# Performance work log

Hardware: AMD Instinct MI355X
Metric: run time of the kernel (lower is better)

## Reference

```python
import jax, jax.numpy as jnp
import numpy as np

# ---- fixed constants from stft2hcfp.__init__ ----
FS = 16000.0; FR = 2.0; FC = 27.5; TC = 1.0 / 4487.0; NPO = 48
N = int(FS / FR)                      # 8000 FFT length
HALF_N = int(round(N / 2))            # 4000
SQRT_N = float(np.sqrt(N))
HIGH_FREQ_IDX = int(round(1.0 / TC / FR) + 1)   # 2245
HIGH_QUEF_IDX = int(round(FS / FC)) + 1         # 583
CUT_Q = int(round(FS * TC))           # 4  (cepstrum cutoff)
TOTAL_BINS = 4 * 88                   # 352 log-freq bins
NUM_HARMONIC = 5

def _central_freqs():
    stop = 1.0 / TC
    nest = int(np.ceil(np.log2(stop / FC)) * NPO)
    cf = []
    for i in range(nest):
        c = FC * 2.0 ** (float(i) / NPO)
        if c < stop:
            cf.append(c)
        else:
            break
    return cf

CF = _central_freqs()   # 353 central frequencies
NEST = len(CF)

def _freq_matrix():
    # triangular log-frequency filterbank over linear freq axis
    f = (FS * np.linspace(0, 0.5, HALF_N, endpoint=True))[:HIGH_FREQ_IDX]
    W = np.zeros((NEST - 1, len(f)), np.float32)
    for i in range(1, NEST - 1):
        l = int(round(CF[i - 1] / FR)); r = int(round(CF[i + 1] / FR) + 1)
        if l >= r - 1:
            W[i, l] = 1.0
        else:
            for j in range(l, r):
                if CF[i - 1] < f[j] < CF[i]:
                    W[i, j] = (f[j] - CF[i - 1]) / (CF[i] - CF[i - 1])
                elif CF[i] < f[j] < CF[i + 1]:
                    W[i, j] = (CF[i + 1] - f[j]) / (CF[i + 1] - CF[i])
    return W

def _quef_matrix():
    q = np.arange(HIGH_QUEF_IDX) / FS + 1e-6
    fq = 1.0 / q
    W = np.zeros((NEST - 1, len(fq)), np.float32)
    for i in range(1, NEST - 1):
        for j in range(int(round(FS / CF[i + 1])), int(round(FS / CF[i - 1]) + 1)):
            if j >= len(fq):
                continue
            if CF[i - 1] < fq[j] < CF[i]:
                W[i, j] = (fq[j] - CF[i - 1]) / (CF[i] - CF[i - 1])
            elif CF[i] < fq[j] < CF[i + 1]:
                W[i, j] = (CF[i + 1] - fq[j]) / (CF[i + 1] - CF[i])
    return W

# harmonic shift indices: closest central freq to (k+1)*27.5 Hz, k=0..5
HIDS = [int(np.argmin(np.abs(np.asarray(CF) - (k + 1) * FC))) for k in range(NUM_HARMONIC + 1)]


def _nonlinear(x, g, cutoff):
    # relu + pow(g), then zero first/last `cutoff` rows along axis 1.
    # safe pow: grad is 0 where x<=0 (matches relu-masked torch behavior, no inf at 0)
    y = jnp.where(x > 0, jnp.where(x > 0, x, 1.0) ** g, 0.0)
    y = y.at[:, :cutoff].set(0.0).at[:, -cutoff:].set(0.0)
    return y


def setup_inputs() -> dict:
    key = jax.random.key(0)
    dx = jax.random.uniform(key, (8, 512, N), dtype=jnp.float32)  # [B, T, 8000] spectrogram
    return {
        "dx": dx,
        "W_freq": jnp.asarray(_freq_matrix()),   # [352, 2245]
        "W_quef": jnp.asarray(_quef_matrix()),   # [352, 583]
    }


def reference(dx, W_freq, W_quef):
    tfr0 = jnp.swapaxes(dx, 1, 2)                       # [B, F=8000, T]
    # CFP layer 1: real part of FFT over freq axis -> cepstrum, nonlinear g=0.6
    ceps = jnp.fft.fft(tfr0, axis=1).real / SQRT_N      # [B, 8000, T]
    ceps = _nonlinear(ceps, 0.6, CUT_Q)
    # log-frequency mappings (banded triangular filterbanks)
    tfr0h = tfr0[:, :HIGH_FREQ_IDX]                      # [B, 2245, T]
    cepsh = ceps[:, :HIGH_QUEF_IDX]                      # [B, 583, T]
    tfrL0 = jnp.einsum('kf,bft->bkt', W_freq, tfr0h)     # [B, 352, T]
    tfrLQ = jnp.einsum('kq,bqt->bkt', W_quef, cepsh)     # [B, 352, T]
    # harmonic stacking: shift down (spectral) / shift up (cepstral)
    har_s = [jnp.pad(tfrL0[:, h:TOTAL_BINS], ((0, 0), (0, h), (0, 0))) for h in HIDS]
    har_c = [jnp.pad(tfrLQ[:, :TOTAL_BINS - h], ((0, 0), (h, 0), (0, 0))) for h in HIDS]
    piece = jnp.concatenate([jnp.stack(har_s, axis=1), jnp.stack(har_c, axis=1)], axis=1)
    return jnp.swapaxes(piece, 2, 3)                     # [B, 12, T, 352]
```

## Files before the change

### kernel.cpp

```cpp
#include <hip/hip_runtime.h>
#include <hip/hip_bf16.h>
#include <limits.h>

typedef __attribute__((ext_vector_type(8))) short short8;
typedef __attribute__((ext_vector_type(4))) float f32x4;

#define NN 8000
#define NCOL 4096
#define KBINS 352
#define QPAD 640
#define QH 160
#define BN 128
#define KC 4
#define NTILE 125
#define CUTQ 4
#define T_ 512
#define WFB 64
#define WQB 20

#define GLL16(g, l) __builtin_amdgcn_global_load_lds( \
    (const __attribute__((address_space(1))) unsigned int*)(g), \
    (__attribute__((address_space(3))) unsigned int*)(l), 16, 0, 0)

static __device__ __forceinline__ ushort bfc(float f){
  __hip_bfloat16 h = __float2bfloat16(f);
  return *reinterpret_cast<ushort*>(&h);
}

__global__ void gen_cos_k(ushort* __restrict__ cosg, int HQI){
  int n = blockIdx.x*256 + threadIdx.x;
  int q = blockIdx.y;
  if (n >= NN) return;
  float v = 0.f;
  if (q < HQI){
    int m = (q*n) % NN;
    v = cosf((float)m * 7.8539816339744831e-4f);
  }
  int kt = n >> 6, s8 = (n >> 3) & 7, e = n & 7;
  cosg[(size_t)kt*(QPAD*64) + (size_t)q*64 + (((s8 ^ (q & 7)) << 3) | e)] = bfc(v);
}

__global__ void bounds_k(const float* __restrict__ W, int width,
                         int* __restrict__ lo, int* __restrict__ hi){
  __shared__ int slo, shi;
  int r = blockIdx.x;
  if (threadIdx.x==0){ slo = INT_MAX; shi = -1; }
  __syncthreads();
  int mylo = INT_MAX, myhi = -1;
  for (int c = threadIdx.x; c < width; c += 256){
    if (W[(size_t)r*width + c] != 0.f){ if (c < mylo) mylo = c; if (c > myhi) myhi = c; }
  }
  atomicMin(&slo, mylo); atomicMax(&shi, myhi);
  __syncthreads();
  if (threadIdx.x==0){
    if (shi < 0){ lo[r] = 0; hi[r] = 0; }
    else        { lo[r] = slo; hi[r] = shi + 1; }
  }
}

__global__ void pack_k(const float* __restrict__ W, const int* __restrict__ lo,
                       const int* __restrict__ hi, int width, int bw,
                       float* __restrict__ WT){
  int r = blockIdx.x;
  int l = lo[r], h = hi[r];
  for (int j = threadIdx.x; j < bw; j += 64){
    float v = 0.f;
    if (l + j < h) v = W[(size_t)r*width + l + j];
    WT[(size_t)j*KBINS + r] = v;
  }
}

__global__ __launch_bounds__(512, 4) void gemm_k(const float* __restrict__ dx,
                                                 const ushort* __restrict__ cosg,
                                                 float* __restrict__ part){
  __shared__ ushort As[2][QH*64];
  __shared__ ushort Bs[2][BN*64];
  int tid = threadIdx.x;
  int nb = blockIdx.x, qh = blockIdx.y, kc = blockIdx.z;
  int lane = tid & 63, widx = tid >> 6;
  int wm = widx & 1, wn = widx >> 1;
  int lrow = lane & 15, lk = lane >> 4;
  int kt0 = kc*32, ktE = (kt0 + 32 < NTILE) ? kt0 + 32 : NTILE;

  int brow = tid >> 2, bfo = (tid & 3) << 4;
  const float* dxp = dx + (size_t)(nb*BN + brow)*NN + bfo;
  int s8a = (tid & 3) << 1;
  const int bo0 = brow*64 + ((s8a ^ (brow & 7)) << 3);
  const int bo1 = brow*64 + (((s8a + 1) ^ (brow & 7)) << 3);
  const ushort* cg0 = cosg + (size_t)qh*(QH*64) + tid*8;

  f32x4 acc[5][2];
  #pragma unroll
  for (int a=0;a<5;a++){ acc[a][0] = (f32x4)0.f; acc[a][1] = (f32x4)0.f; }

  f32x4 d0,d1,d2,d3;
  {
    const float* p = dxp + (size_t)kt0*64;
    d0 = *(const f32x4*)p; d1 = *(const f32x4*)(p+4);
    d2 = *(const f32x4*)(p+8); d3 = *(const f32x4*)(p+12);
  }
  {
    const ushort* cg = cg0 + (size_t)kt0*(QPAD*64);
    GLL16(cg,        &As[0][tid*8]);
    GLL16(cg + 4096, &As[0][4096 + tid*8]);
    if (tid < 256) GLL16(cg + 8192, &As[0][8192 + tid*8]);
    short8 a8, b8;
    a8[0]=(short)bfc(d0[0]); a8[1]=(short)bfc(d0[1]); a8[2]=(short)bfc(d0[2]); a8[3]=(short)bfc(d0[3]);
    a8[4]=(short)bfc(d1[0]); a8[5]=(short)bfc(d1[1]); a8[6]=(short)bfc(d1[2]); a8[7]=(short)bfc(d1[3]);
    b8[0]=(short)bfc(d2[0]); b8[1]=(short)bfc(d2[1]); b8[2]=(short)bfc(d2[2]); b8[3]=(short)bfc(d2[3]);
    b8[4]=(short)bfc(d3[0]); b8[5]=(short)bfc(d3[1]); b8[6]=(short)bfc(d3[2]); b8[7]=(short)bfc(d3[3]);
    *(short8*)(&Bs[0][bo0]) = a8;
    *(short8*)(&Bs[0][bo1]) = b8;
    if (kt0 + 1 < ktE){
      const float* p = dxp + (size_t)(kt0+1)*64;
      d0 = *(const f32x4*)p; d1 = *(const f32x4*)(p+4);
      d2 = *(const f32x4*)(p+8); d3 = *(const f32x4*)(p+12);
    }
  }
  __syncthreads();

  int cur = 0;
  for (int kt = kt0; kt < ktE; ++kt){
    if (kt + 1 < ktE){
      const ushort* cg = cg0 + (size_t)(kt+1)*(QPAD*64);
      ushort* an = &As[cur^1][0];
      GLL16(cg,        an + tid*8);
      GLL16(cg + 4096, an + 4096 + tid*8);
      if (tid < 256) GLL16(cg + 8192, an + 8192 + tid*8);
      short8 a8, b8;
      a8[0]=(short)bfc(d0[0]); a8[1]=(short)bfc(d0[1]); a8[2]=(short)bfc(d0[2]); a8[3]=(short)bfc(d0[3]);
      a8[4]=(short)bfc(d1[0]); a8[5]=(short)bfc(d1[1]); a8[6]=(short)bfc(d1[2]); a8[7]=(short)bfc(d1[3]);
      b8[0]=(short)bfc(d2[0]); b8[1]=(short)bfc(d2[1]); b8[2]=(short)bfc(d2[2]); b8[3]=(short)bfc(d2[3]);
      b8[4]=(short)bfc(d3[0]); b8[5]=(short)bfc(d3[1]); b8[6]=(short)bfc(d3[2]); b8[7]=(short)bfc(d3[3]);
      ushort* bn = &Bs[cur^1][0];
      *(short8*)(bn + bo0) = a8;
      *(short8*)(bn + bo1) = b8;
      if (kt + 2 < ktE){
        const float* p = dxp + (size_t)(kt+2)*64;
        d0 = *(const f32x4*)p; d1 = *(const f32x4*)(p+4);
        d2 = *(const f32x4*)(p+8); d3 = *(const f32x4*)(p+12);
      }
    }
    const ushort* Ac = &As[cur][0];
    const ushort* Bc = &Bs[cur][0];
    #pragma unroll
    for (int p=0;p<2;p++){
      short8 bfrag[5];
      #pragma unroll
      for (int a=0;a<5;a++){
        int row = wm*80 + 16*a + lrow;
        bfrag[a] = *(const short8*)(Ac + row*64 + ((((p<<2)|lk) ^ (row & 7)) << 3));
      }
      short8 afr[2];
      #pragma unroll
      for (int c=0;c<2;c++){
        int row = wn*32 + 16*c + lrow;
        afr[c] = *(const short8*)(Bc + row*64 + ((((p<<2)|lk) ^ (row & 7)) << 3));
      }
      #pragma unroll
      for (int a=0;a<5;a++){
        acc[a][0] = __builtin_amdgcn_mfma_f32_16x16x32_bf16(afr[0], bfrag[a], acc[a][0], 0,0,0);
        acc[a][1] = __builtin_amdgcn_mfma_f32_16x16x32_bf16(afr[1], bfrag[a], acc[a][1], 0,0,0);
      }
    }
    __syncthreads();
    cur ^= 1;
  }

  float* pb = part + (size_t)kc*NCOL*QPAD;
  #pragma unroll
  for (int a=0;a<5;a++){
    int q = qh*QH + wm*80 + 16*a + lrow;
    #pragma unroll
    for (int c=0;c<2;c++){
      int col = nb*BN + wn*32 + 16*c + 4*lk;
      #pragma unroll
      for (int r=0;r<4;r++) pb[(size_t)(col+r)*QPAD + q] = acc[a][c][r];
    }
  }
}

__global__ __launch_bounds__(384) void fuse_k(const float* __restrict__ dx,
        const float* __restrict__ part,
        const float* __restrict__ WfT, const float* __restrict__ WqT,
        const int* __restrict__ fLo, const int* __restrict__ qLo,
        float* __restrict__ out, int HFI, int HQI){
  __shared__ float xr[2304];
  __shared__ float yq[QPAD];
  __shared__ float tl0[KBINS];
  __shared__ float tlq[KBINS];
  int col = blockIdx.x;
  int b = col >> 9, t = col & 511;
  int tid = threadIdx.x;
  const float invs = 0.011180339887498949f;

  for (int f = tid; f < 2304; f += 384) xr[f] = (f < HFI) ? dx[(size_t)col*NN + f] : 0.f;
  for (int q = tid; q < QPAD; q += 384){
    float y = 0.f;
    if (q < HQI){
      float s = 0.f;
      #pragma unroll
      for (int kc=0; kc<KC; kc++) s += part[(size_t)kc*NCOL*QPAD + (size_t)col*QPAD + q];
      s *= invs;
      if (q >= CUTQ && s > 0.f) y = powf(s, 0.6f);
    }
    yq[q] = y;
  }
  __syncthreads();

  if (tid < KBINS){
    int k = tid;
    int lo = fLo[k];
    float aF = 0.f;
    #pragma unroll
    for (int j=0;j<WFB;j++) aF += WfT[j*KBINS + k] * xr[lo + j];
    int ql = qLo[k];
    float aQ = 0.f;
    #pragma unroll
    for (int j=0;j<WQB;j++) aQ += WqT[j*KBINS + k] * yq[ql + j];
    tl0[k] = aF; tlq[k] = aQ;
  }
  __syncthreads();

  const int hids[6] = {0,48,76,96,111,124};
  for (int u = tid; u < 12*KBINS; u += 384){
    int j = u / KBINS;
    int k = u - j*KBINS;
    int h = hids[(j < 6) ? j : j - 6];
    float v;
    if (j < 6) v = (k + h < KBINS) ? tl0[k + h] : 0.f;
    else       v = (k >= h)        ? tlq[k - h] : 0.f;
    out[(((size_t)b*12 + j)*T_ + t)*KBINS + k] = v;
  }
}

extern "C" void kernel_launch(void* const* d_in, const int* in_sizes, int n_in,
                              void* d_out, int out_size, void* d_ws, size_t ws_size,
                              hipStream_t stream){
  const float* dx = (const float*)d_in[0];
  const float* Wf = (const float*)d_in[1];
  const float* Wq = (const float*)d_in[2];
  int HFI = in_sizes[1] / KBINS;
  int HQI = in_sizes[2] / KBINS;
  float* out = (float*)d_out;
  char* ws = (char*)d_ws;

  ushort* cosg = (ushort*)ws;
  size_t off = (size_t)NTILE*QPAD*64*2;
  float* part = (float*)(ws + off); off += (size_t)KC*NCOL*QPAD*4;
  int* fLo = (int*)(ws+off); off += KBINS*4;
  int* fHi = (int*)(ws+off); off += KBINS*4;
  int* qLo = (int*)(ws+off); off += KBINS*4;
  int* qHi = (int*)(ws+off); off += KBINS*4;
  float* WfT = (float*)(ws+off); off += (size_t)WFB*KBINS*4;
  float* WqT = (float*)(ws+off); off += (size_t)WQB*KBINS*4;
  (void)n_in; (void)out_size; (void)ws_size;

  gen_cos_k<<<dim3((NN+255)/256, QPAD), 256, 0, stream>>>(cosg, HQI);
  bounds_k<<<KBINS, 256, 0, stream>>>(Wf, HFI, fLo, fHi);
  bounds_k<<<KBINS, 256, 0, stream>>>(Wq, HQI, qLo, qHi);
  pack_k<<<KBINS, 64, 0, stream>>>(Wf, fLo, fHi, HFI, WFB, WfT);
  pack_k<<<KBINS, 64, 0, stream>>>(Wq, qLo, qHi, HQI, WQB, WqT);
  gemm_k<<<dim3(NCOL/BN, QPAD/QH, KC), 512, 0, stream>>>(dx, cosg, part);
  fuse_k<<<NCOL, 384, 0, stream>>>(dx, part, WfT, WqT, fLo, qLo, out, HFI, HQI);
}
```

Baseline: 142.0 us.

## Enlarge GEMM tiles, use 32x32 MFMA, and store bf16 split-K partials

The cosine-transform GEMM now uses larger tiles (320 quefrency rows by 256 columns) with 32x32x16 bf16 MFMA instructions and 8-way split-K instead of 4. The dx tile write to LDS moves after the MFMA loop so the global loads can overlap compute. Partial sums are stored as bf16, halving partial-buffer traffic, and fuse_k reads and reduces eight bf16 partials. The aim is more operand reuse per LDS load and less memory traffic, at the cost of lower occupancy (launch bounds 2), more accumulator registers, and extra rounding error in the partials. The fuse_k xr buffer is also widened.

```diff
diff --git a/kernel.cpp b/kernel.cpp
--- a/kernel.cpp
+++ b/kernel.cpp
@@ -3,15 +3,17 @@
 #include <limits.h>
 
 typedef __attribute__((ext_vector_type(8))) short short8;
+typedef __attribute__((ext_vector_type(4))) short short4v;
 typedef __attribute__((ext_vector_type(4))) float f32x4;
+typedef __attribute__((ext_vector_type(16))) float f32x16;
 
 #define NN 8000
 #define NCOL 4096
 #define KBINS 352
 #define QPAD 640
-#define QH 160
-#define BN 128
-#define KC 4
+#define QH 320
+#define BN 256
+#define KC 8
 #define NTILE 125
 #define CUTQ 4
 #define T_ 512
@@ -25,6 +27,9 @@
 static __device__ __forceinline__ ushort bfc(float f){
   __hip_bfloat16 h = __float2bfloat16(f);
   return *reinterpret_cast<ushort*>(&h);
+}
+static __device__ __forceinline__ float b2f(ushort u){
+  unsigned v = ((unsigned)u) << 16; float f; __builtin_memcpy(&f, &v, 4); return f;
 }
 
 __global__ void gen_cos_k(ushort* __restrict__ cosg, int HQI){
@@ -70,122 +75,100 @@
   }
 }
 
-__global__ __launch_bounds__(512, 4) void gemm_k(const float* __restrict__ dx,
+__global__ __launch_bounds__(512, 2) void gemm_k(const float* __restrict__ dx,
                                                  const ushort* __restrict__ cosg,
-                                                 float* __restrict__ part){
+                                                 ushort* __restrict__ part){
   __shared__ ushort As[2][QH*64];
   __shared__ ushort Bs[2][BN*64];
   int tid = threadIdx.x;
   int nb = blockIdx.x, qh = blockIdx.y, kc = blockIdx.z;
   int lane = tid & 63, widx = tid >> 6;
   int wm = widx & 1, wn = widx >> 1;
-  int lrow = lane & 15, lk = lane >> 4;
-  int kt0 = kc*32, ktE = (kt0 + 32 < NTILE) ? kt0 + 32 : NTILE;
-
-  int brow = tid >> 2, bfo = (tid & 3) << 4;
-  const float* dxp = dx + (size_t)(nb*BN + brow)*NN + bfo;
-  int s8a = (tid & 3) << 1;
-  const int bo0 = brow*64 + ((s8a ^ (brow & 7)) << 3);
-  const int bo1 = brow*64 + (((s8a + 1) ^ (brow & 7)) << 3);
-  const ushort* cg0 = cosg + (size_t)qh*(QH*64) + tid*8;
-
-  f32x4 acc[5][2];
+  int l31 = lane & 31, lh = lane >> 5;
+  int kt0 = kc*16, ktE = (kc < 7) ? kt0 + 16 : NTILE;
+
+  int srow = widx*4 + (lane >> 4);
+  int sfo  = (lane & 15) * 4;
+  int slot16 = (lane & 15) >> 1, shalf = (lane & 15) & 1;
+  const ushort* cg0 = cosg + (size_t)qh*(QH*64);
+
+  f32x16 acc[5][2];
   #pragma unroll
-  for (int a=0;a<5;a++){ acc[a][0] = (f32x4)0.f; acc[a][1] = (f32x4)0.f; }
-
-  f32x4 d0,d1,d2,d3;
-  {
-    const float* p = dxp + (size_t)kt0*64;
-    d0 = *(const f32x4*)p; d1 = *(const f32x4*)(p+4);
-    d2 = *(const f32x4*)(p+8); d3 = *(const f32x4*)(p+12);
-  }
-  {
-    const ushort* cg = cg0 + (size_t)kt0*(QPAD*64);
-    GLL16(cg,        &As[0][tid*8]);
-    GLL16(cg + 4096, &As[0][4096 + tid*8]);
-    if (tid < 256) GLL16(cg + 8192, &As[0][8192 + tid*8]);
-    short8 a8, b8;
-    a8[0]=(short)bfc(d0[0]); a8[1]=(short)bfc(d0[1]); a8[2]=(short)bfc(d0[2]); a8[3]=(short)bfc(d0[3]);
-    a8[4]=(short)bfc(d1[0]); a8[5]=(short)bfc(d1[1]); a8[6]=(short)bfc(d1[2]); a8[7]=(short)bfc(d1[3]);
-    b8[0]=(short)bfc(d2[0]); b8[1]=(short)bfc(d2[1]); b8[2]=(short)bfc(d2[2]); b8[3]=(short)bfc(d2[3]);
-    b8[4]=(short)bfc(d3[0]); b8[5]=(short)bfc(d3[1]); b8[6]=(short)bfc(d3[2]); b8[7]=(short)bfc(d3[3]);
-    *(short8*)(&Bs[0][bo0]) = a8;
-    *(short8*)(&Bs[0][bo1]) = b8;
-    if (kt0 + 1 < ktE){
-      const float* p = dxp + (size_t)(kt0+1)*64;
-      d0 = *(const f32x4*)p; d1 = *(const f32x4*)(p+4);
-      d2 = *(const f32x4*)(p+8); d3 = *(const f32x4*)(p+12);
-    }
-  }
+  for (int a=0;a<5;a++){ acc[a][0] = (f32x16)0.f; acc[a][1] = (f32x16)0.f; }
+
+  f32x4 d[8];
+  #define DX_LOAD(kt_) { _Pragma("unroll") \
+    for (int i=0;i<8;i++){ int row = i*32 + srow; \
+      d[i] = *(const f32x4*)(dx + (size_t)(nb*BN + row)*NN + (size_t)(kt_)*64 + sfo); } }
+  #define DX_WRITE(buf) { _Pragma("unroll") \
+    for (int i=0;i<8;i++){ int row = i*32 + srow; \
+      short4v s; s[0]=(short)bfc(d[i][0]); s[1]=(short)bfc(d[i][1]); \
+                 s[2]=(short)bfc(d[i][2]); s[3]=(short)bfc(d[i][3]); \
+      *(short4v*)(&Bs[buf][row*64 + (((slot16 ^ (row & 7)) << 3) | (shalf << 2))]) = s; } }
+  #define COS_STAGE(kt_, buf) { const ushort* cg = cg0 + (size_t)(kt_)*(QPAD*64) + tid*8; \
+    _Pragma("unroll") \
+    for (int i=0;i<5;i++) GLL16(cg + i*4096, &As[buf][i*4096 + tid*8]); }
+
+  DX_LOAD(kt0);
+  COS_STAGE(kt0, 0);
+  DX_WRITE(0);
   __syncthreads();
 
   int cur = 0;
   for (int kt = kt0; kt < ktE; ++kt){
     if (kt + 1 < ktE){
-      const ushort* cg = cg0 + (size_t)(kt+1)*(QPAD*64);
-      ushort* an = &As[cur^1][0];
-      GLL16(cg,        an + tid*8);
-      GLL16(cg + 4096, an + 4096 + tid*8);
-      if (tid < 256) GLL16(cg + 8192, an + 8192 + tid*8);
-      short8 a8, b8;
-      a8[0]=(short)bfc(d0[0]); a8[1]=(short)bfc(d0[1]); a8[2]=(short)bfc(d0[2]); a8[3]=(short)bfc(d0[3]);
-      a8[4]=(short)bfc(d1[0]); a8[5]=(short)bfc(d1[1]); a8[6]=(short)bfc(d1[2]); a8[7]=(short)bfc(d1[3]);
-      b8[0]=(short)bfc(d2[0]); b8[1]=(short)bfc(d2[1]); b8[2]=(short)bfc(d2[2]); b8[3]=(short)bfc(d2[3]);
-      b8[4]=(short)bfc(d3[0]); b8[5]=(short)bfc(d3[1]); b8[6]=(short)bfc(d3[2]); b8[7]=(short)bfc(d3[3]);
-      ushort* bn = &Bs[cur^1][0];
-      *(short8*)(bn + bo0) = a8;
-      *(short8*)(bn + bo1) = b8;
-      if (kt + 2 < ktE){
-        const float* p = dxp + (size_t)(kt+2)*64;
-        d0 = *(const f32x4*)p; d1 = *(const f32x4*)(p+4);
-        d2 = *(const f32x4*)(p+8); d3 = *(const f32x4*)(p+12);
-      }
+      COS_STAGE(kt+1, cur^1);
+      DX_LOAD(kt+1);
     }
     const ushort* Ac = &As[cur][0];
     const ushort* Bc = &Bs[cur][0];
     #pragma unroll
-    for (int p=0;p<2;p++){
-      short8 bfrag[5];
+    for (int p=0;p<4;p++){
+      short8 dfr[2];
+      #pragma unroll
+      for (int c=0;c<2;c++){
+        int row = wn*64 + c*32 + l31;
+        dfr[c] = *(const short8*)(Bc + row*64 + ((((p<<1)|lh) ^ (row & 7)) << 3));
+      }
+      short8 cfr[5];
       #pragma unroll
       for (int a=0;a<5;a++){
-        int row = wm*80 + 16*a + lrow;
-        bfrag[a] = *(const short8*)(Ac + row*64 + ((((p<<2)|lk) ^ (row & 7)) << 3));
-      }
-      short8 afr[2];
-      #pragma unroll
-      for (int c=0;c<2;c++){
-        int row = wn*32 + 16*c + lrow;
-        afr[c] = *(const short8*)(Bc + row*64 + ((((p<<2)|lk) ^ (row & 7)) << 3));
+        int row = wm*160 + a*32 + l31;
+        cfr[a] = *(const short8*)(Ac + row*64 + ((((p<<1)|lh) ^ (row & 7)) << 3));
       }
       #pragma unroll
       for (int a=0;a<5;a++){
-        acc[a][0] = __builtin_amdgcn_mfma_f32_16x16x32_bf16(afr[0], bfrag[a], acc[a][0], 0,0,0);
-        acc[a][1] = __builtin_amdgcn_mfma_f32_16x16x32_bf16(afr[1], bfrag[a], acc[a][1], 0,0,0);
-      }
-    }
+        acc[a][0] = __builtin_amdgcn_mfma_f32_32x32x16_bf16(dfr[0], cfr[a], acc[a][0], 0,0,0);
+        acc[a][1] = __builtin_amdgcn_mfma_f32_32x32x16_bf16(dfr[1], cfr[a], acc[a][1], 0,0,0);
+      }
+    }
+    if (kt + 1 < ktE) DX_WRITE(cur^1);
     __syncthreads();
     cur ^= 1;
   }
 
-  float* pb = part + (size_t)kc*NCOL*QPAD;
+  ushort* pb = part + (size_t)kc*NCOL*QPAD;
   #pragma unroll
   for (int a=0;a<5;a++){
-    int q = qh*QH + wm*80 + 16*a + lrow;
+    int q = qh*QH + wm*160 + a*32 + l31;
     #pragma unroll
     for (int c=0;c<2;c++){
-      int col = nb*BN + wn*32 + 16*c + 4*lk;
-      #pragma unroll
-      for (int r=0;r<4;r++) pb[(size_t)(col+r)*QPAD + q] = acc[a][c][r];
+      int colb = nb*BN + wn*64 + c*32 + 4*lh;
+      #pragma unroll
+      for (int r=0;r<16;r++){
+        int col = colb + (r&3) + 8*(r>>2);
+        pb[(size_t)col*QPAD + q] = bfc(acc[a][c][r]);
+      }
     }
   }
 }
 
 __global__ __launch_bounds__(384) void fuse_k(const float* __restrict__ dx,
-        const float* __restrict__ part,
+        const ushort* __restrict__ part,
         const float* __restrict__ WfT, const float* __restrict__ WqT,
         const int* __restrict__ fLo, const int* __restrict__ qLo,
         float* __restrict__ out, int HFI, int HQI){
-  __shared__ float xr[2304];
+  __shared__ float xr[2368];
   __shared__ float yq[QPAD];
   __shared__ float tl0[KBINS];
   __shared__ float tlq[KBINS];
@@ -194,13 +177,14 @@
   int tid = threadIdx.x;
   const float invs = 0.011180339887498949f;
 
-  for (int f = tid; f < 2304; f += 384) xr[f] = (f < HFI) ? dx[(size_t)col*NN + f] : 0.f;
+  for (int f = tid; f < 2368; f += 384) xr[f] = (f < HFI) ? dx[(size_t)col*NN + f] : 0.f;
+  const ushort* pc = part + (size_t)col*QPAD;
   for (int q = tid; q < QPAD; q += 384){
     float y = 0.f;
     if (q < HQI){
       float s = 0.f;
       #pragma unroll
-      for (int kc=0; kc<KC; kc++) s += part[(size_t)kc*NCOL*QPAD + (size_t)col*QPAD + q];
+      for (int kc=0; kc<KC; kc++) s += b2f(pc[(size_t)kc*NCOL*QPAD + q]);
       s *= invs;
       if (q >= CUTQ && s > 0.f) y = powf(s, 0.6f);
     }
@@ -247,7 +231,7 @@
 
   ushort* cosg = (ushort*)ws;
   size_t off = (size_t)NTILE*QPAD*64*2;
-  float* part = (float*)(ws + off); off += (size_t)KC*NCOL*QPAD*4;
+  ushort* part = (ushort*)(ws + off); off += (size_t)KC*NCOL*QPAD*2;
   int* fLo = (int*)(ws+off); off += KBINS*4;
   int* fHi = (int*)(ws+off); off += KBINS*4;
   int* qLo = (int*)(ws+off); off += KBINS*4;
```

Measured after the change: 139.7 us. No clear change (-1.6%).
